# Optimization experiments

Hardware: AMD Instinct MI355X
Metric: run time of the kernel (lower is better)

Reference implementation:

```python
import jax, jax.numpy as jnp
import numpy as np

N_NODES = 50000
N_EDGES = 600000
IN_DIM = 128
HID_DIM = 256
LAT_DIM = 64


def setup_inputs() -> dict:
    key = jax.random.key(0)
    k_x, k_e, k_w1, k_b1, k_w2, k_b2 = jax.random.split(key, 6)
    x = jax.random.normal(k_x, (N_NODES, IN_DIM), dtype=jnp.float32)
    edge_index = jax.random.randint(k_e, (2, N_EDGES), 0, N_NODES, dtype=jnp.int64)
    # torch nn.Linear default init: U(-1/sqrt(fan_in), 1/sqrt(fan_in))
    lim1 = 1.0 / np.sqrt(2 * IN_DIM)
    lim2 = 1.0 / np.sqrt(HID_DIM)
    W1 = jax.random.uniform(k_w1, (2 * IN_DIM, HID_DIM), jnp.float32, -lim1, lim1)
    b1 = jax.random.uniform(k_b1, (HID_DIM,), jnp.float32, -lim1, lim1)
    W2 = jax.random.uniform(k_w2, (HID_DIM, LAT_DIM), jnp.float32, -lim2, lim2)
    b2 = jax.random.uniform(k_b2, (LAT_DIM,), jnp.float32, -lim2, lim2)
    return {"x": x, "edge_index": edge_index, "W1": W1, "b1": b1, "W2": W2, "b2": b2}


def reference(x, edge_index, W1, b1, W2, b2):
    h_i = x[edge_index[0]]                     # [E, D]
    h_j = x[edge_index[1]]                     # [E, D]
    edge_features = jnp.concatenate([h_i, h_j], axis=-1)  # [E, 2D]
    hidden = jax.nn.relu(edge_features @ W1 + b1)          # [E, H]
    return hidden @ W2 + b2                                # [E, L]
```

## Files before the change

### kernel.cpp

```cpp
#include <hip/hip_runtime.h>

#define E_TOTAL 600000
#define NT2 4688
#define LDH 264

typedef __attribute__((ext_vector_type(8))) short short8;
typedef __attribute__((ext_vector_type(4))) short short4v;
typedef __attribute__((ext_vector_type(4))) float f32x4;

__device__ __forceinline__ unsigned f2bf_u(float f) {
  union { float f; unsigned u; } v; v.f = f;
  return (v.u + 0x7fffu + ((v.u >> 16) & 1u)) >> 16;
}

__device__ __forceinline__ void ldsBarrier() {
  asm volatile("s_waitcnt lgkmcnt(0)\n\ts_barrier" ::: "memory");
}

__global__ __launch_bounds__(256) void prep_weights(
    const float* __restrict__ W1, const float* __restrict__ W2,
    unsigned short* __restrict__ W1t, unsigned short* __restrict__ W2t) {
  __shared__ float t[32][33];
  int bid = blockIdx.x;
  const float* S; unsigned short* D; int k0, n0, N;
  if (bid < 64) { S = W1; D = W1t; N = 256; k0 = (bid >> 3) * 32; n0 = (bid & 7) * 32; }
  else { bid -= 64; S = W2; D = W2t; N = 64; k0 = (bid >> 1) * 32; n0 = (bid & 1) * 32; }
  int tx = threadIdx.x & 31, ty = threadIdx.x >> 5;
#pragma unroll
  for (int i = 0; i < 32; i += 8) t[ty + i][tx] = S[(k0 + ty + i) * N + n0 + tx];
  __syncthreads();
#pragma unroll
  for (int i = 0; i < 32; i += 8)
    D[(n0 + ty + i) * 256 + k0 + tx] = (unsigned short)f2bf_u(t[tx][ty + i]);
}

__global__ __launch_bounds__(256) void prep_x(const float* __restrict__ x,
                                              unsigned short* __restrict__ xb) {
  int i = (blockIdx.x * 256 + threadIdx.x) * 4;
  f32x4 v = *(const f32x4*)(x + i);
  short4v s;
#pragma unroll
  for (int j = 0; j < 4; ++j) s[j] = (short)f2bf_u(v[j]);
  *(short4v*)(xb + i) = s;
}

__global__ __launch_bounds__(256, 2) void edge_mlp(
    const unsigned short* __restrict__ xb, const int* __restrict__ ei,
    const unsigned short* __restrict__ W1t, const unsigned short* __restrict__ W2t,
    const float* __restrict__ b1, const float* __restrict__ b2,
    float* __restrict__ out) {
  __shared__ __align__(16) unsigned short lds[128 * LDH];
  __shared__ float ldsb1[256];
  __shared__ float ldsb2[64];

  const int tid = threadIdx.x;
  const int base = blockIdx.x * 128;
  const int* __restrict__ srcI = ei;
  const int* __restrict__ dstI = ei + E_TOTAL;

  const int lane = tid & 63;
  const int w = tid >> 6;
  const int m = lane & 15;
  const int q = lane >> 4;

  const int kb = (tid & 31) * 8;
  const int xo = kb & 127;
  const int e0 = tid >> 5;
  const int* __restrict__ idxp = (kb < 128) ? srcI : dstI;

  int nodes[16];
#pragma unroll
  for (int i = 0; i < 16; ++i) {
    int e = base + e0 + 8 * i;
    nodes[i] = idxp[e < E_TOTAL ? e : (E_TOTAL - 1)];
  }

  float b2tmp = 0.f;
  if (tid < 64) b2tmp = b2[tid];
  float b1tmp = b1[tid];
  ldsb1[tid] = b1tmp;
  if (tid < 64) ldsb2[tid] = b2tmp;

#pragma unroll
  for (int i = 0; i < 16; ++i) {
    const unsigned short* p = xb + nodes[i] * 128 + xo;
    short8 v = *(const short8*)p;
    *(short8*)&lds[(e0 + 8 * i) * LDH + kb] = v;
  }

  int w1off[4];
#pragma unroll
  for (int nt = 0; nt < 4; ++nt) w1off[nt] = ((w * 4 + nt) * 16 + m) * 256 + q * 8;
  const int w2off = (w * 16 + m) * 256 + q * 8;

  short8 wa[2][4];
#pragma unroll
  for (int nt = 0; nt < 4; ++nt) wa[0][nt] = *(const short8*)&W1t[w1off[nt]];

  ldsBarrier();

  f32x4 acc[4][8];
#pragma unroll
  for (int nt = 0; nt < 4; ++nt)
#pragma unroll
    for (int mt = 0; mt < 8; ++mt) acc[nt][mt] = (f32x4){0.f, 0.f, 0.f, 0.f};

#pragma unroll
  for (int kk = 0; kk < 8; ++kk) {
    const int cur = kk & 1, nx = cur ^ 1;
    if (kk < 7) {
#pragma unroll
      for (int nt = 0; nt < 4; ++nt)
        wa[nx][nt] = *(const short8*)&W1t[w1off[nt] + (kk + 1) * 32];
    }
    short8 f[8];
#pragma unroll
    for (int mt = 0; mt < 8; ++mt)
      f[mt] = *(const short8*)&lds[(mt * 16 + m) * LDH + kk * 32 + q * 8];
#pragma unroll
    for (int nt = 0; nt < 4; ++nt)
#pragma unroll
      for (int mt = 0; mt < 8; ++mt)
        acc[nt][mt] = __builtin_amdgcn_mfma_f32_16x16x32_bf16(wa[cur][nt], f[mt], acc[nt][mt], 0, 0, 0);
  }

  ldsBarrier();

  short8 w2f[8];
#pragma unroll
  for (int j = 0; j < 8; ++j) w2f[j] = *(const short8*)&W2t[w2off + j * 32];

  f32x4 bias[4];
#pragma unroll
  for (int nt = 0; nt < 4; ++nt) bias[nt] = *(const f32x4*)&ldsb1[w * 64 + nt * 16 + q * 4];
#pragma unroll
  for (int nt = 0; nt < 4; ++nt)
#pragma unroll
    for (int mt = 0; mt < 8; ++mt) {
      float h0 = fmaxf(acc[nt][mt][0] + bias[nt][0], 0.f);
      float h1 = fmaxf(acc[nt][mt][1] + bias[nt][1], 0.f);
      float h2 = fmaxf(acc[nt][mt][2] + bias[nt][2], 0.f);
      float h3 = fmaxf(acc[nt][mt][3] + bias[nt][3], 0.f);
      uint2 pk;
      pk.x = f2bf_u(h0) | (f2bf_u(h1) << 16);
      pk.y = f2bf_u(h2) | (f2bf_u(h3) << 16);
      *(uint2*)&lds[(mt * 16 + m) * LDH + w * 64 + nt * 16 + q * 4] = pk;
    }

  ldsBarrier();

  f32x4 acc2[8];
#pragma unroll
  for (int mt = 0; mt < 8; ++mt) acc2[mt] = (f32x4){0.f, 0.f, 0.f, 0.f};
#pragma unroll
  for (int kk = 0; kk < 8; ++kk) {
#pragma unroll
    for (int mt = 0; mt < 8; ++mt) {
      short8 h = *(const short8*)&lds[(mt * 16 + m) * LDH + kk * 32 + q * 8];
      acc2[mt] = __builtin_amdgcn_mfma_f32_16x16x32_bf16(w2f[kk], h, acc2[mt], 0, 0, 0);
    }
  }

  f32x4 b2v = *(const f32x4*)&ldsb2[w * 16 + q * 4];
#pragma unroll
  for (int mt = 0; mt < 8; ++mt) {
    int e = base + mt * 16 + m;
    if (e < E_TOTAL) {
      f32x4 o;
#pragma unroll
      for (int r = 0; r < 4; ++r) o[r] = acc2[mt][r] + b2v[r];
      *(f32x4*)&out[e * 64 + w * 16 + q * 4] = o;
    }
  }
}

extern "C" void kernel_launch(void* const* d_in, const int* in_sizes, int n_in,
                              void* d_out, int out_size, void* d_ws, size_t ws_size,
                              hipStream_t stream) {
  const float* x  = (const float*)d_in[0];
  const int*   ei = (const int*)d_in[1];
  const float* W1 = (const float*)d_in[2];
  const float* b1 = (const float*)d_in[3];
  const float* W2 = (const float*)d_in[4];
  const float* b2 = (const float*)d_in[5];
  float* out = (float*)d_out;

  unsigned short* W1t = (unsigned short*)d_ws;
  unsigned short* W2t = W1t + 256 * 256;
  unsigned short* xb  = W2t + 64 * 256;

  prep_weights<<<80, 256, 0, stream>>>(W1, W2, W1t, W2t);
  prep_x<<<6250, 256, 0, stream>>>(x, xb);
  edge_mlp<<<NT2, 256, 0, stream>>>(xb, ei, W1t, W2t, b1, b2, out);
}
```

Before: 328.0 us.

## Precompute per-node first-layer projections and gather them per edge

```diff
diff --git a/kernel.cpp b/kernel.cpp
--- a/kernel.cpp
+++ b/kernel.cpp
@@ -1,103 +1,89 @@
 #include <hip/hip_runtime.h>
 
 #define E_TOTAL 600000
-#define NT2 4688
-#define LDH 264
+#define N_NODES 50000
+#define ETILE 96
+#define NETILES 6250
+#define NNT 391
+#define LDH2 136
+#define LDH3 264
 
 typedef __attribute__((ext_vector_type(8))) short short8;
-typedef __attribute__((ext_vector_type(4))) short short4v;
+typedef __attribute__((ext_vector_type(8))) _Float16 half8;
 typedef __attribute__((ext_vector_type(4))) float f32x4;
 
 __device__ __forceinline__ unsigned f2bf_u(float f) {
   union { float f; unsigned u; } v; v.f = f;
   return (v.u + 0x7fffu + ((v.u >> 16) & 1u)) >> 16;
 }
-
-__device__ __forceinline__ void ldsBarrier() {
-  asm volatile("s_waitcnt lgkmcnt(0)\n\ts_barrier" ::: "memory");
-}
-
-__global__ __launch_bounds__(256) void prep_weights(
+__device__ __forceinline__ unsigned short f2h_u(float f) {
+  union { _Float16 h; unsigned short u; } v; v.h = (_Float16)f;
+  return v.u;
+}
+
+__global__ __launch_bounds__(256) void prep(
     const float* __restrict__ W1, const float* __restrict__ W2,
-    unsigned short* __restrict__ W1t, unsigned short* __restrict__ W2t) {
+    const float* __restrict__ b1,
+    unsigned short* __restrict__ W1c, unsigned short* __restrict__ W2t2,
+    unsigned short* __restrict__ b1h) {
   __shared__ float t[32][33];
   int bid = blockIdx.x;
-  const float* S; unsigned short* D; int k0, n0, N;
-  if (bid < 64) { S = W1; D = W1t; N = 256; k0 = (bid >> 3) * 32; n0 = (bid & 7) * 32; }
-  else { bid -= 64; S = W2; D = W2t; N = 64; k0 = (bid >> 1) * 32; n0 = (bid & 1) * 32; }
   int tx = threadIdx.x & 31, ty = threadIdx.x >> 5;
-#pragma unroll
-  for (int i = 0; i < 32; i += 8) t[ty + i][tx] = S[(k0 + ty + i) * N + n0 + tx];
+  if (bid < 64) {
+    int k0 = (bid >> 3) * 32, n0 = (bid & 7) * 32;
+#pragma unroll
+    for (int i = 0; i < 32; i += 8) t[ty + i][tx] = W1[(k0 + ty + i) * 256 + n0 + tx];
+    __syncthreads();
+    int coff = (k0 >= 128) ? 256 : 0;
+#pragma unroll
+    for (int i = 0; i < 32; i += 8)
+      W1c[(n0 + ty + i + coff) * 128 + (k0 & 127) + tx] = (unsigned short)f2bf_u(t[tx][ty + i]);
+  } else if (bid < 80) {
+    int b = bid - 64;
+    int k0 = (b >> 1) * 32, n0 = (b & 1) * 32;
+#pragma unroll
+    for (int i = 0; i < 32; i += 8) t[ty + i][tx] = W2[(k0 + ty + i) * 64 + n0 + tx];
+    __syncthreads();
+#pragma unroll
+    for (int i = 0; i < 32; i += 8)
+      W2t2[(n0 + ty + i) * 256 + k0 + tx] = f2h_u(t[tx][ty + i]);
+  } else {
+    b1h[threadIdx.x] = f2h_u(b1[threadIdx.x]);
+  }
+}
+
+__global__ __launch_bounds__(256, 2) void node_uv(
+    const float* __restrict__ x, const unsigned short* __restrict__ W1c,
+    unsigned short* __restrict__ UV) {
+  __shared__ __align__(16) unsigned short xt[128 * LDH2];
+  const int tid = threadIdx.x;
+  const int bid = blockIdx.x;
+  const int ntile = bid >> 1, chalf = bid & 1;
+  const int n0 = ntile * 128;
+  const int lane = tid & 63, w = tid >> 6, m = lane & 15, q = lane >> 4;
+
+  const int kb = (tid & 15) * 8;
+  const int e0 = tid >> 4;
+#pragma unroll
+  for (int i = 0; i < 8; ++i) {
+    int r = e0 + 16 * i;
+    int n = n0 + r; if (n >= N_NODES) n = N_NODES - 1;
+    const float* p = x + n * 128 + kb;
+    f32x4 g0 = *(const f32x4*)p, g1 = *(const f32x4*)(p + 4);
+    short8 s;
+#pragma unroll
+    for (int j = 0; j < 4; ++j) { s[j] = (short)f2bf_u(g0[j]); s[4 + j] = (short)f2bf_u(g1[j]); }
+    *(short8*)&xt[r * LDH2 + kb] = s;
+  }
+
+  int w1o[4];
+#pragma unroll
+  for (int nt = 0; nt < 4; ++nt) w1o[nt] = (chalf * 256 + (w * 4 + nt) * 16 + m) * 128 + q * 8;
+  short8 wa[2][4];
+#pragma unroll
+  for (int nt = 0; nt < 4; ++nt) wa[0][nt] = *(const short8*)&W1c[w1o[nt]];
+
   __syncthreads();
-#pragma unroll
-  for (int i = 0; i < 32; i += 8)
-    D[(n0 + ty + i) * 256 + k0 + tx] = (unsigned short)f2bf_u(t[tx][ty + i]);
-}
-
-__global__ __launch_bounds__(256) void prep_x(const float* __restrict__ x,
-                                              unsigned short* __restrict__ xb) {
-  int i = (blockIdx.x * 256 + threadIdx.x) * 4;
-  f32x4 v = *(const f32x4*)(x + i);
-  short4v s;
-#pragma unroll
-  for (int j = 0; j < 4; ++j) s[j] = (short)f2bf_u(v[j]);
-  *(short4v*)(xb + i) = s;
-}
-
-__global__ __launch_bounds__(256, 2) void edge_mlp(
-    const unsigned short* __restrict__ xb, const int* __restrict__ ei,
-    const unsigned short* __restrict__ W1t, const unsigned short* __restrict__ W2t,
-    const float* __restrict__ b1, const float* __restrict__ b2,
-    float* __restrict__ out) {
-  __shared__ __align__(16) unsigned short lds[128 * LDH];
-  __shared__ float ldsb1[256];
-  __shared__ float ldsb2[64];
-
-  const int tid = threadIdx.x;
-  const int base = blockIdx.x * 128;
-  const int* __restrict__ srcI = ei;
-  const int* __restrict__ dstI = ei + E_TOTAL;
-
-  const int lane = tid & 63;
-  const int w = tid >> 6;
-  const int m = lane & 15;
-  const int q = lane >> 4;
-
-  const int kb = (tid & 31) * 8;
-  const int xo = kb & 127;
-  const int e0 = tid >> 5;
-  const int* __restrict__ idxp = (kb < 128) ? srcI : dstI;
-
-  int nodes[16];
-#pragma unroll
-  for (int i = 0; i < 16; ++i) {
-    int e = base + e0 + 8 * i;
-    nodes[i] = idxp[e < E_TOTAL ? e : (E_TOTAL - 1)];
-  }
-
-  float b2tmp = 0.f;
-  if (tid < 64) b2tmp = b2[tid];
-  float b1tmp = b1[tid];
-  ldsb1[tid] = b1tmp;
-  if (tid < 64) ldsb2[tid] = b2tmp;
-
-#pragma unroll
-  for (int i = 0; i < 16; ++i) {
-    const unsigned short* p = xb + nodes[i] * 128 + xo;
-    short8 v = *(const short8*)p;
-    *(short8*)&lds[(e0 + 8 * i) * LDH + kb] = v;
-  }
-
-  int w1off[4];
-#pragma unroll
-  for (int nt = 0; nt < 4; ++nt) w1off[nt] = ((w * 4 + nt) * 16 + m) * 256 + q * 8;
-  const int w2off = (w * 16 + m) * 256 + q * 8;
-
-  short8 wa[2][4];
-#pragma unroll
-  for (int nt = 0; nt < 4; ++nt) wa[0][nt] = *(const short8*)&W1t[w1off[nt]];
-
-  ldsBarrier();
 
   f32x4 acc[4][8];
 #pragma unroll
@@ -106,17 +92,16 @@
     for (int mt = 0; mt < 8; ++mt) acc[nt][mt] = (f32x4){0.f, 0.f, 0.f, 0.f};
 
 #pragma unroll
-  for (int kk = 0; kk < 8; ++kk) {
+  for (int kk = 0; kk < 4; ++kk) {
     const int cur = kk & 1, nx = cur ^ 1;
-    if (kk < 7) {
-#pragma unroll
-      for (int nt = 0; nt < 4; ++nt)
-        wa[nx][nt] = *(const short8*)&W1t[w1off[nt] + (kk + 1) * 32];
+    if (kk < 3) {
+#pragma unroll
+      for (int nt = 0; nt < 4; ++nt) wa[nx][nt] = *(const short8*)&W1c[w1o[nt] + (kk + 1) * 32];
     }
     short8 f[8];
 #pragma unroll
     for (int mt = 0; mt < 8; ++mt)
-      f[mt] = *(const short8*)&lds[(mt * 16 + m) * LDH + kk * 32 + q * 8];
+      f[mt] = *(const short8*)&xt[(mt * 16 + m) * LDH2 + kk * 32 + q * 8];
 #pragma unroll
     for (int nt = 0; nt < 4; ++nt)
 #pragma unroll
@@ -124,53 +109,85 @@
         acc[nt][mt] = __builtin_amdgcn_mfma_f32_16x16x32_bf16(wa[cur][nt], f[mt], acc[nt][mt], 0, 0, 0);
   }
 
-  ldsBarrier();
-
-  short8 w2f[8];
-#pragma unroll
-  for (int j = 0; j < 8; ++j) w2f[j] = *(const short8*)&W2t[w2off + j * 32];
-
-  f32x4 bias[4];
-#pragma unroll
-  for (int nt = 0; nt < 4; ++nt) bias[nt] = *(const f32x4*)&ldsb1[w * 64 + nt * 16 + q * 4];
 #pragma unroll
   for (int nt = 0; nt < 4; ++nt)
 #pragma unroll
     for (int mt = 0; mt < 8; ++mt) {
-      float h0 = fmaxf(acc[nt][mt][0] + bias[nt][0], 0.f);
-      float h1 = fmaxf(acc[nt][mt][1] + bias[nt][1], 0.f);
-      float h2 = fmaxf(acc[nt][mt][2] + bias[nt][2], 0.f);
-      float h3 = fmaxf(acc[nt][mt][3] + bias[nt][3], 0.f);
-      uint2 pk;
-      pk.x = f2bf_u(h0) | (f2bf_u(h1) << 16);
-      pk.y = f2bf_u(h2) | (f2bf_u(h3) << 16);
-      *(uint2*)&lds[(mt * 16 + m) * LDH + w * 64 + nt * 16 + q * 4] = pk;
-    }
-
-  ldsBarrier();
-
-  f32x4 acc2[8];
-#pragma unroll
-  for (int mt = 0; mt < 8; ++mt) acc2[mt] = (f32x4){0.f, 0.f, 0.f, 0.f};
+      int n = n0 + mt * 16 + m;
+      if (n < N_NODES) {
+        union { _Float16 h[4]; uint2 u; } pk;
+#pragma unroll
+        for (int r = 0; r < 4; ++r) pk.h[r] = (_Float16)acc[nt][mt][r];
+        *(uint2*)&UV[n * 512 + chalf * 256 + w * 64 + nt * 16 + q * 4] = pk.u;
+      }
+    }
+}
+
+__global__ __launch_bounds__(256, 2) void edge_mlp(
+    const unsigned short* __restrict__ UV, const int* __restrict__ ei,
+    const unsigned short* __restrict__ W2t2, const unsigned short* __restrict__ b1h,
+    const float* __restrict__ b2, float* __restrict__ out) {
+  __shared__ __align__(16) unsigned short hid[ETILE * LDH3];
+  const int tid = threadIdx.x;
+  const int base = blockIdx.x * ETILE;
+  const int lane = tid & 63, w = tid >> 6, m = lane & 15, q = lane >> 4;
+  const int c = tid & 31;
+  const int e0 = tid >> 5;
+
+  half8 w2r[8];
+  const int w2off = (w * 16 + m) * 256 + q * 8;
+#pragma unroll
+  for (int kk = 0; kk < 8; ++kk) w2r[kk] = *(const half8*)&W2t2[w2off + kk * 32];
+  half8 bias = *(const half8*)&b1h[c * 8];
+  f32x4 b2v = *(const f32x4*)&b2[w * 16 + q * 4];
+
+  int si[12], di[12];
+#pragma unroll
+  for (int i = 0; i < 12; ++i) {
+    int e = base + e0 + 8 * i;
+    si[i] = ei[e];
+    di[i] = ei[E_TOTAL + e];
+  }
+
+#pragma unroll
+  for (int g = 0; g < 2; ++g) {
+    half8 lu[6], lv[6];
+#pragma unroll
+    for (int i = 0; i < 6; ++i) {
+      const int r = g * 6 + i;
+      lu[i] = *(const half8*)&UV[(size_t)si[r] * 512 + c * 8];
+      lv[i] = *(const half8*)&UV[(size_t)di[r] * 512 + 256 + c * 8];
+    }
+#pragma unroll
+    for (int i = 0; i < 6; ++i) {
+      const int r = g * 6 + i;
+      half8 s = lu[i] + lv[i] + bias;
+#pragma unroll
+      for (int j = 0; j < 8; ++j) s[j] = s[j] > (_Float16)0 ? s[j] : (_Float16)0;
+      *(half8*)&hid[(e0 + 8 * r) * LDH3 + c * 8] = s;
+    }
+  }
+
+  __syncthreads();
+
+  f32x4 acc2[6];
+#pragma unroll
+  for (int mt = 0; mt < 6; ++mt) acc2[mt] = (f32x4){0.f, 0.f, 0.f, 0.f};
 #pragma unroll
   for (int kk = 0; kk < 8; ++kk) {
 #pragma unroll
-    for (int mt = 0; mt < 8; ++mt) {
-      short8 h = *(const short8*)&lds[(mt * 16 + m) * LDH + kk * 32 + q * 8];
-      acc2[mt] = __builtin_amdgcn_mfma_f32_16x16x32_bf16(w2f[kk], h, acc2[mt], 0, 0, 0);
-    }
-  }
-
-  f32x4 b2v = *(const f32x4*)&ldsb2[w * 16 + q * 4];
-#pragma unroll
-  for (int mt = 0; mt < 8; ++mt) {
-    int e = base + mt * 16 + m;
-    if (e < E_TOTAL) {
-      f32x4 o;
-#pragma unroll
-      for (int r = 0; r < 4; ++r) o[r] = acc2[mt][r] + b2v[r];
-      *(f32x4*)&out[e * 64 + w * 16 + q * 4] = o;
-    }
+    for (int mt = 0; mt < 6; ++mt) {
+      half8 h = *(const half8*)&hid[(mt * 16 + m) * LDH3 + kk * 32 + q * 8];
+      acc2[mt] = __builtin_amdgcn_mfma_f32_16x16x32_f16(w2r[kk], h, acc2[mt], 0, 0, 0);
+    }
+  }
+
+#pragma unroll
+  for (int mt = 0; mt < 6; ++mt) {
+    f32x4 o;
+#pragma unroll
+    for (int r = 0; r < 4; ++r) o[r] = acc2[mt][r] + b2v[r];
+    __builtin_nontemporal_store(o, (f32x4*)&out[(size_t)(base + mt * 16 + m) * 64 + w * 16 + q * 4]);
   }
 }
 
@@ -185,11 +202,12 @@
   const float* b2 = (const float*)d_in[5];
   float* out = (float*)d_out;
 
-  unsigned short* W1t = (unsigned short*)d_ws;
-  unsigned short* W2t = W1t + 256 * 256;
-  unsigned short* xb  = W2t + 64 * 256;
-
-  prep_weights<<<80, 256, 0, stream>>>(W1, W2, W1t, W2t);
-  prep_x<<<6250, 256, 0, stream>>>(x, xb);
-  edge_mlp<<<NT2, 256, 0, stream>>>(xb, ei, W1t, W2t, b1, b2, out);
-}
+  unsigned short* W1c  = (unsigned short*)d_ws;
+  unsigned short* W2t2 = W1c + 512 * 128;
+  unsigned short* b1h  = W2t2 + 64 * 256;
+  unsigned short* UV   = b1h + 256;
+
+  prep<<<81, 256, 0, stream>>>(W1, W2, b1, W1c, W2t2, b1h);
+  node_uv<<<NNT * 2, 256, 0, stream>>>(x, W1c, UV);
+  edge_mlp<<<NETILES, 256, 0, stream>>>(UV, ei, W2t2, b1h, b2, out);
+}
```

New measurement: 304.9 us. -7.0%, faster.
